# Optimization experiments

Measured on AMD Instinct MI355X. Metric: run time of the kernel, lower is better.

The kernel has to match this reference:

```python
import jax, jax.numpy as jnp
import numpy as np

SCALE_WEIGHT = 0.5 ** 0.5
B, C, T, S = 8, 512, 2048, 2048


def setup_inputs() -> dict:
    key = jax.random.key(0)
    ks = jax.random.split(key, 6)
    return {
        "base_target_emb": jax.random.normal(ks[0], (B, C, T, 1), dtype=jnp.float32),
        "input_from_dec": jax.random.normal(ks[1], (B, C, T, 1), dtype=jnp.float32),
        "encoder_out_top": jax.random.normal(ks[2], (B, C, S), dtype=jnp.float32),
        "encoder_out_combine": jax.random.normal(ks[3], (B, C, S), dtype=jnp.float32),
        "W": jax.random.normal(ks[4], (C, C), dtype=jnp.float32) * (1.0 / np.sqrt(C)),
        "b": jax.random.normal(ks[5], (C,), dtype=jnp.float32) * 0.01,
    }


def reference(base_target_emb, input_from_dec, encoder_out_top, encoder_out_combine, W, b):
    # seq_linear: per-token Linear over the channel dim. torch Linear: h = x @ W.T + b, W is [out,in]
    x = input_from_dec[..., 0]                                # [B,C,T]
    preatt = jnp.einsum('oc,bct->bot', W, x) + b[None, :, None]  # [B,C,T]
    target = (base_target_emb[..., 0] + preatt) * SCALE_WEIGHT   # [B,C,T]
    pre_attn = jnp.einsum('bct,bcs->bts', target, encoder_out_top)  # [B,T,S]
    attn = jax.nn.softmax(pre_attn, axis=2)                      # [B,T,S]
    ctx = jnp.einsum('bts,bcs->btc', attn, encoder_out_combine)  # [B,T,C]
    context_output = jnp.transpose(ctx, (0, 2, 1))[..., None]    # [B,C,T,1]
    return context_output, attn
```

## Files before the change

### kernel.cpp

```cpp
#include <hip/hip_runtime.h>
#include <cstddef>
#include <cstdint>

#define SCALE_WEIGHT 0.70710678118654752440f

static constexpr int B_ = 8, C_ = 512, T_ = 2048, S_ = 2048;
static constexpr size_t BCT_ = (size_t)B_ * C_ * T_;
static constexpr size_t BTS_ = (size_t)B_ * T_ * S_;

typedef _Float16 half_t;
typedef half_t half8  __attribute__((ext_vector_type(8)));
typedef half_t half4v __attribute__((ext_vector_type(4)));
typedef float  floatx4 __attribute__((ext_vector_type(4)));

__device__ __forceinline__ void gload_lds16(const void* g, void* l) {
    __builtin_amdgcn_global_load_lds(
        (const __attribute__((address_space(1))) void*)g,
        (__attribute__((address_space(3))) void*)l, 16, 0, 0);
}

__global__ __launch_bounds__(256) void transpose2_cvt_kernel(
    const float* __restrict__ x, const float* __restrict__ top,
    half_t* __restrict__ xT, half_t* __restrict__ topT)
{
    __shared__ float tile[64][65];
    const int z = blockIdx.z;
    const float* in = (z < 8) ? x : top;
    half_t* outp = (z < 8) ? xT : topT;
    const int b  = z & 7;
    const int r0 = blockIdx.y * 64, c0 = blockIdx.x * 64;
    const float* ib = in + (size_t)b * C_ * T_;
    half_t* ob = outp + (size_t)b * C_ * T_;
    const int t  = threadIdx.x;
    const int rr = t >> 4, cq = t & 15;
    #pragma unroll
    for (int i = 0; i < 4; ++i) {
        const int r = rr + i * 16;
        float4 v = *(const float4*)&ib[(size_t)(r0 + r) * T_ + c0 + cq * 4];
        tile[cq * 4 + 0][r] = v.x;
        tile[cq * 4 + 1][r] = v.y;
        tile[cq * 4 + 2][r] = v.z;
        tile[cq * 4 + 3][r] = v.w;
    }
    __syncthreads();
    const int cw = t >> 4, rq = (t & 15) * 4;
    #pragma unroll
    for (int i = 0; i < 4; ++i) {
        const int c = cw + i * 16;
        half4v h = {(half_t)tile[c][rq + 0], (half_t)tile[c][rq + 1],
                    (half_t)tile[c][rq + 2], (half_t)tile[c][rq + 3]};
        *(half4v*)&ob[(size_t)(c0 + c) * C_ + r0 + rq] = h;
    }
}

__global__ __launch_bounds__(256) void cvt2_f32_f16_kernel(
    const float* __restrict__ comb, half_t* __restrict__ combh,
    const float* __restrict__ W, half_t* __restrict__ Wh,
    int n4a, int n4tot)
{
    const int stride = gridDim.x * blockDim.x;
    for (int i = blockIdx.x * blockDim.x + threadIdx.x; i < n4tot; i += stride) {
        const float4* src; half4v* dst; int j;
        if (i < n4a) { src = (const float4*)comb; dst = (half4v*)combh; j = i; }
        else         { src = (const float4*)W;    dst = (half4v*)Wh;    j = i - n4a; }
        float4 v = src[j];
        dst[j] = (half4v){(half_t)v.x, (half_t)v.y, (half_t)v.z, (half_t)v.w};
    }
}

template<int MM, int NN, int KK, int EPI>
__global__ __launch_bounds__(256) void gemm32_kernel(
    const half_t* __restrict__ A, const half_t* __restrict__ Bm,
    size_t sA, size_t sB,
    float* __restrict__ outF, half_t* __restrict__ outH,
    const float* __restrict__ base, const float* __restrict__ bias,
    float* __restrict__ mArr, float* __restrict__ sArr,
    const float* __restrict__ fArr)
{
    constexpr int LDSSZ = (EPI == 1) ? 34816 : ((EPI == 2) ? 40960 : 32768);
    __shared__ __align__(128) char smem[LDSSZ];

    const int tid = threadIdx.x, lane = tid & 63, w = tid >> 6;
    const int wr = w >> 1, wc = w & 1;

    const int wgid = blockIdx.x;
    const int b = wgid & 7;
    const int tile = wgid >> 3;
    constexpr int NXT = NN / 128;
    constexpr int NMT = MM / 128;
    int m0, n0;
    if constexpr (EPI == 2) { n0 = (tile / NMT) * 128; m0 = (tile % NMT) * 128; }
    else                    { n0 = (tile % NXT) * 128; m0 = (tile / NXT) * 128; }

    const half_t* Ab = A  + (size_t)b * sA;
    const half_t* Bb = Bm + (size_t)b * sB;

    const int lr = lane >> 2, sl = lane & 3;
    const int ks = sl ^ (lr & 3);
    const half_t* aG0 = Ab + (size_t)(m0 + w * 32      + lr) * KK + ks * 8;
    const half_t* aG1 = Ab + (size_t)(m0 + w * 32 + 16 + lr) * KK + ks * 8;
    const half_t* bG0 = Bb + (size_t)(n0 + w * 32      + lr) * KK + ks * 8;
    const half_t* bG1 = Bb + (size_t)(n0 + w * 32 + 16 + lr) * KK + ks * 8;
    const int dOff0 = (w * 32) * 64, dOff1 = (w * 32 + 16) * 64;

    const int fr = lane & 15, kg = lane >> 4;
    const int q4 = kg * 4;
    int aoff[4], boff[4];
    #pragma unroll
    for (int mi = 0; mi < 4; ++mi) {
        const int m = wr * 64 + mi * 16 + fr;
        aoff[mi] = m * 64 + ((kg ^ (m & 3)) << 4);
    }
    #pragma unroll
    for (int nj = 0; nj < 4; ++nj) {
        const int n = wc * 64 + nj * 16 + fr;
        boff[nj] = n * 64 + ((kg ^ (n & 3)) << 4);
    }

    floatx4 acc[4][4];
    #pragma unroll
    for (int mi = 0; mi < 4; ++mi)
        #pragma unroll
        for (int nj = 0; nj < 4; ++nj)
            acc[mi][nj] = (floatx4){0.f, 0.f, 0.f, 0.f};

    auto STAGE = [&](int t, int pg) {
        const int k0 = t * 32;
        char* Ad = smem + pg * 8192;
        char* Bd = smem + 16384 + pg * 8192;
        gload_lds16(aG0 + k0, Ad + dOff0);
        gload_lds16(aG1 + k0, Ad + dOff1);
        gload_lds16(bG0 + k0, Bd + dOff0);
        gload_lds16(bG1 + k0, Bd + dOff1);
    };

    auto COMPUTE = [&](int pg, int t) {
        const char* Ar = smem + pg * 8192;
        const char* Br = smem + 16384 + pg * 8192;
        half8 af[4], bf[4];
        #pragma unroll
        for (int mi = 0; mi < 4; ++mi) af[mi] = *(const half8*)(Ar + aoff[mi]);
        #pragma unroll
        for (int nj = 0; nj < 4; ++nj) bf[nj] = *(const half8*)(Br + boff[nj]);
        if constexpr (EPI == 2) {
            const float* fls = (const float*)(smem + 32768);
            const int st = t >> 2;
            #pragma unroll
            for (int nj = 0; nj < 4; ++nj) {
                const half_t fh = (half_t)fls[st * 128 + wc * 64 + nj * 16 + fr];
                #pragma unroll
                for (int e = 0; e < 8; ++e) bf[nj][e] *= fh;
            }
        }
        #pragma unroll
        for (int mi = 0; mi < 4; ++mi)
            #pragma unroll
            for (int nj = 0; nj < 4; ++nj)
                acc[mi][nj] = __builtin_amdgcn_mfma_f32_16x16x32_f16(
                    af[mi], bf[nj], acc[mi][nj], 0, 0, 0);
    };

    if constexpr (EPI == 2) {
        const float* fB = fArr + (size_t)b * 16 * T_;
        #pragma unroll
        for (int c = 0; c < 8; ++c)
            gload_lds16(fB + (size_t)(2 * c + (lane >> 5)) * T_ + n0 + (lane & 31) * 4,
                        smem + 32768 + c * 1024);
    }
    constexpr int NT = KK / 32;
    STAGE(0, 0);
    int cur = 0;
    #pragma unroll 1
    for (int t = 0; t < NT - 1; ++t) {
        STAGE(t + 1, cur ^ 1);
        __builtin_amdgcn_sched_barrier(0);
        asm volatile("s_waitcnt vmcnt(4)" ::: "memory");
        __builtin_amdgcn_s_barrier();
        __builtin_amdgcn_sched_barrier(0);
        COMPUTE(cur, t);
        asm volatile("s_waitcnt lgkmcnt(0)" ::: "memory");
        __builtin_amdgcn_sched_barrier(0);
        __builtin_amdgcn_s_barrier();
        __builtin_amdgcn_sched_barrier(0);
        cur ^= 1;
    }
    asm volatile("s_waitcnt vmcnt(0)" ::: "memory");
    __builtin_amdgcn_s_barrier();
    __builtin_amdgcn_sched_barrier(0);
    COMPUTE(cur, NT - 1);

    if constexpr (EPI == 0) {
        half_t* Cb = outH + (size_t)b * ((size_t)MM * NN);
        #pragma unroll
        for (int nj = 0; nj < 4; ++nj) {
            const int col = n0 + wc * 64 + nj * 16 + fr;
            const float bn = bias[col];
            const float* bp = base + ((size_t)b * NN + col) * (size_t)MM;
            #pragma unroll
            for (int mi = 0; mi < 4; ++mi) {
                const int row = m0 + wr * 64 + mi * 16 + q4;
                #pragma unroll
                for (int r = 0; r < 4; ++r) {
                    float v = (acc[mi][nj][r] + bn + bp[row + r]) * SCALE_WEIGHT;
                    Cb[(size_t)(row + r) * NN + col] = (half_t)v;
                }
            }
        }
    } else if constexpr (EPI == 2) {
        float* Cb = outF + (size_t)b * ((size_t)MM * NN);
        #pragma unroll
        for (int mi = 0; mi < 4; ++mi) {
            const int row = m0 + wr * 64 + mi * 16 + q4;
            #pragma unroll
            for (int nj = 0; nj < 4; ++nj) {
                const int col = n0 + wc * 64 + nj * 16 + fr;
                #pragma unroll
                for (int r = 0; r < 4; ++r)
                    Cb[(size_t)(row + r) * NN + col] = acc[mi][nj][r];
            }
        }
    } else {
        __syncthreads();
        float* rmax = (float*)(smem + 32768);
        float* rsum = (float*)(smem + 32768 + 1024);

        #pragma unroll
        for (int mi = 0; mi < 4; ++mi)
            #pragma unroll
            for (int r = 0; r < 4; ++r) {
                float v = fmaxf(fmaxf(acc[mi][0][r], acc[mi][1][r]),
                                fmaxf(acc[mi][2][r], acc[mi][3][r]));
                v = fmaxf(v, __shfl_xor(v, 1));
                v = fmaxf(v, __shfl_xor(v, 2));
                v = fmaxf(v, __shfl_xor(v, 4));
                v = fmaxf(v, __shfl_xor(v, 8));
                if (fr == 0) rmax[wc * 128 + wr * 64 + mi * 16 + q4 + r] = v;
            }
        __syncthreads();

        #pragma unroll
        for (int mi = 0; mi < 4; ++mi)
            #pragma unroll
            for (int r = 0; r < 4; ++r) {
                const int row = wr * 64 + mi * 16 + q4 + r;
                const float mC = fmaxf(rmax[row], rmax[128 + row]);
                float s = 0.f;
                #pragma unroll
                for (int nj = 0; nj < 4; ++nj) {
                    const int col = wc * 64 + nj * 16 + fr;
                    float pv = __expf(acc[mi][nj][r] - mC);
                    s += pv;
                    *(half_t*)(smem + row * 256 + ((col * 2) ^ ((row & 7) << 4))) =
                        (half_t)pv;
                }
                s += __shfl_xor(s, 1);
                s += __shfl_xor(s, 2);
                s += __shfl_xor(s, 4);
                s += __shfl_xor(s, 8);
                if (fr == 0) rsum[wc * 128 + row] = s;
            }
        __syncthreads();

        if (tid < 128) {
            const float m = fmaxf(rmax[tid], rmax[128 + tid]);
            const float s = rsum[tid] + rsum[128 + tid];
            const size_t si = ((size_t)(b * 16 + (n0 >> 7))) * (size_t)MM + m0 + tid;
            mArr[si] = m;
            sArr[si] = s;
        }

        half_t* Pb = outH + ((size_t)b * MM + m0) * (size_t)NN + n0;
        const int rlo = tid >> 4, slot = tid & 15;
        #pragma unroll
        for (int pp = 0; pp < 8; ++pp) {
            const int row = pp * 16 + rlo;
            const int lb = row * 256 + ((slot * 16) ^ ((row & 7) << 4));
            half8 v = *(const half8*)(smem + lb);
            *(half8*)&Pb[(size_t)row * NN + slot * 8] = v;
        }
    }
}

__global__ __launch_bounds__(256) void kf_kernel(
    const float* __restrict__ mArr, const float* __restrict__ sArr,
    float* __restrict__ fArr)
{
    const int gid = blockIdx.x * 256 + threadIdx.x;
    const int b = gid >> 11, t = gid & 2047;
    float mv[16];
    float mfin = -3.0e38f;
    #pragma unroll
    for (int j = 0; j < 16; ++j) {
        mv[j] = mArr[((size_t)(b * 16 + j)) * T_ + t];
        mfin = fmaxf(mfin, mv[j]);
    }
    float sig = 0.f;
    #pragma unroll
    for (int j = 0; j < 16; ++j)
        sig += sArr[((size_t)(b * 16 + j)) * T_ + t] * __expf(mv[j] - mfin);
    const float inv = 1.f / sig;
    #pragma unroll
    for (int j = 0; j < 16; ++j)
        fArr[((size_t)(b * 16 + j)) * T_ + t] = __expf(mv[j] - mfin) * inv;
}

__global__ __launch_bounds__(256) void k3n_kernel(
    const half_t* __restrict__ P, const float* __restrict__ fArr,
    float* __restrict__ attnf)
{
    const int bid = blockIdx.x;
    const int b = bid >> 11, t = bid & 2047;
    const int tid = threadIdx.x;
    const float f = fArr[((size_t)(b * 16 + (tid >> 4))) * T_ + t];
    const size_t rb = (size_t)bid * S_ + tid * 8;
    half8 v = *(const half8*)&P[rb];
    float4 o0 = {(float)v[0] * f, (float)v[1] * f, (float)v[2] * f, (float)v[3] * f};
    float4 o1 = {(float)v[4] * f, (float)v[5] * f, (float)v[6] * f, (float)v[7] * f};
    *(float4*)&attnf[rb]     = o0;
    *(float4*)&attnf[rb + 4] = o1;
}

extern "C" void kernel_launch(void* const* d_in, const int* in_sizes, int n_in,
                              void* d_out, int out_size, void* d_ws, size_t ws_size,
                              hipStream_t stream) {
    const float* base = (const float*)d_in[0];
    const float* x    = (const float*)d_in[1];
    const float* top  = (const float*)d_in[2];
    const float* comb = (const float*)d_in[3];
    const float* W    = (const float*)d_in[4];
    const float* bias = (const float*)d_in[5];

    float* out   = (float*)d_out;
    float* ctx   = out;
    float* attnf = out + BCT_;

    half_t* xT   = (half_t*)d_out;
    half_t* topT = xT + BCT_;

    half_t* pws   = (half_t*)d_ws;
    half_t* combh = pws + BTS_;
    half_t* Wh    = combh + (size_t)B_ * C_ * S_;
    half_t* tgtT  = Wh + (size_t)C_ * C_;
    float*  mArr  = (float*)(tgtT + BCT_);
    float*  sArr  = mArr + (size_t)B_ * 16 * T_;
    float*  fArr  = sArr + (size_t)B_ * 16 * T_;

    transpose2_cvt_kernel<<<dim3(T_ / 64, C_ / 64, 16), 256, 0, stream>>>(x, top, xT, topT);
    {
        const int n4a = (int)((size_t)B_ * C_ * S_ / 4);
        const int n4tot = n4a + C_ * C_ / 4;
        cvt2_f32_f16_kernel<<<2048, 256, 0, stream>>>(comb, combh, W, Wh, n4a, n4tot);
    }

    gemm32_kernel<2048, 512, 512, 0><<<512, 256, 0, stream>>>(
        xT, Wh, (size_t)T_ * C_, 0,
        nullptr, tgtT, base, bias, nullptr, nullptr, nullptr);

    gemm32_kernel<2048, 2048, 512, 1><<<2048, 256, 0, stream>>>(
        tgtT, topT, (size_t)T_ * C_, (size_t)S_ * C_,
        nullptr, pws, nullptr, nullptr, mArr, sArr, nullptr);

    kf_kernel<<<64, 256, 0, stream>>>(mArr, sArr, fArr);

    k3n_kernel<<<B_ * T_, 256, 0, stream>>>(pws, fArr, attnf);

    gemm32_kernel<512, 2048, 2048, 2><<<512, 256, 0, stream>>>(
        combh, pws, (size_t)C_ * S_, (size_t)T_ * S_,
        ctx, nullptr, nullptr, nullptr, nullptr, nullptr, fArr);
}
```

Measured before the change: 235.2 us.

## Enlarge GEMM tiles to 512 threads with 4-stage LDS ring, merge prep kernels

The GEMM kernel now uses 512-thread workgroups with BN=256 and BM=128 or 256, which halves the softmax partial-statistics slices from 16 to 8 per row. The old double-buffered LDS loop is replaced by a 4-deep prefetch ring that needs only one barrier per K step, and MFMA sections are wrapped in s_setprio. The two conversion kernels are merged into one launch. Larger tiles raise data reuse, but they also raise LDS and register pressure and cut the number of workgroups, so occupancy may drop.

```diff
diff --git a/kernel.cpp b/kernel.cpp
--- a/kernel.cpp
+++ b/kernel.cpp
@@ -19,57 +19,58 @@
         (__attribute__((address_space(3))) void*)l, 16, 0, 0);
 }
 
-__global__ __launch_bounds__(256) void transpose2_cvt_kernel(
+__global__ __launch_bounds__(256) void pre_kernel(
     const float* __restrict__ x, const float* __restrict__ top,
-    half_t* __restrict__ xT, half_t* __restrict__ topT)
+    const float* __restrict__ comb, const float* __restrict__ W,
+    half_t* __restrict__ xT, half_t* __restrict__ topT,
+    half_t* __restrict__ combh, half_t* __restrict__ Wh)
 {
-    __shared__ float tile[64][65];
     const int z = blockIdx.z;
-    const float* in = (z < 8) ? x : top;
-    half_t* outp = (z < 8) ? xT : topT;
-    const int b  = z & 7;
-    const int r0 = blockIdx.y * 64, c0 = blockIdx.x * 64;
-    const float* ib = in + (size_t)b * C_ * T_;
-    half_t* ob = outp + (size_t)b * C_ * T_;
-    const int t  = threadIdx.x;
-    const int rr = t >> 4, cq = t & 15;
-    #pragma unroll
-    for (int i = 0; i < 4; ++i) {
-        const int r = rr + i * 16;
-        float4 v = *(const float4*)&ib[(size_t)(r0 + r) * T_ + c0 + cq * 4];
-        tile[cq * 4 + 0][r] = v.x;
-        tile[cq * 4 + 1][r] = v.y;
-        tile[cq * 4 + 2][r] = v.z;
-        tile[cq * 4 + 3][r] = v.w;
-    }
-    __syncthreads();
-    const int cw = t >> 4, rq = (t & 15) * 4;
-    #pragma unroll
-    for (int i = 0; i < 4; ++i) {
-        const int c = cw + i * 16;
-        half4v h = {(half_t)tile[c][rq + 0], (half_t)tile[c][rq + 1],
-                    (half_t)tile[c][rq + 2], (half_t)tile[c][rq + 3]};
-        *(half4v*)&ob[(size_t)(c0 + c) * C_ + r0 + rq] = h;
-    }
-}
-
-__global__ __launch_bounds__(256) void cvt2_f32_f16_kernel(
-    const float* __restrict__ comb, half_t* __restrict__ combh,
-    const float* __restrict__ W, half_t* __restrict__ Wh,
-    int n4a, int n4tot)
-{
-    const int stride = gridDim.x * blockDim.x;
-    for (int i = blockIdx.x * blockDim.x + threadIdx.x; i < n4tot; i += stride) {
-        const float4* src; half4v* dst; int j;
-        if (i < n4a) { src = (const float4*)comb; dst = (half4v*)combh; j = i; }
-        else         { src = (const float4*)W;    dst = (half4v*)Wh;    j = i - n4a; }
-        float4 v = src[j];
-        dst[j] = (half4v){(half_t)v.x, (half_t)v.y, (half_t)v.z, (half_t)v.w};
-    }
-}
-
-template<int MM, int NN, int KK, int EPI>
-__global__ __launch_bounds__(256) void gemm32_kernel(
+    if (z < 16) {
+        __shared__ float tile[64][65];
+        const float* in = (z < 8) ? x : top;
+        half_t* outp = (z < 8) ? xT : topT;
+        const int b  = z & 7;
+        const int r0 = blockIdx.y * 64, c0 = blockIdx.x * 64;
+        const float* ib = in + (size_t)b * C_ * T_;
+        half_t* ob = outp + (size_t)b * C_ * T_;
+        const int t  = threadIdx.x;
+        const int rr = t >> 4, cq = t & 15;
+        #pragma unroll
+        for (int i = 0; i < 4; ++i) {
+            const int r = rr + i * 16;
+            float4 v = *(const float4*)&ib[(size_t)(r0 + r) * T_ + c0 + cq * 4];
+            tile[cq * 4 + 0][r] = v.x;
+            tile[cq * 4 + 1][r] = v.y;
+            tile[cq * 4 + 2][r] = v.z;
+            tile[cq * 4 + 3][r] = v.w;
+        }
+        __syncthreads();
+        const int cw = t >> 4, rq = (t & 15) * 4;
+        #pragma unroll
+        for (int i = 0; i < 4; ++i) {
+            const int c = cw + i * 16;
+            half4v h = {(half_t)tile[c][rq + 0], (half_t)tile[c][rq + 1],
+                        (half_t)tile[c][rq + 2], (half_t)tile[c][rq + 3]};
+            *(half4v*)&ob[(size_t)(c0 + c) * C_ + r0 + rq] = h;
+        }
+    } else {
+        const int n4a = (int)((size_t)B_ * C_ * S_ / 4);
+        const int n4tot = n4a + C_ * C_ / 4;
+        const int planeT = 32 * 8 * 256;
+        for (int i = (blockIdx.y * 32 + blockIdx.x) * 256 + threadIdx.x;
+             i < n4tot; i += planeT) {
+            const float4* src; half4v* dst; int j;
+            if (i < n4a) { src = (const float4*)comb; dst = (half4v*)combh; j = i; }
+            else         { src = (const float4*)W;    dst = (half4v*)Wh;    j = i - n4a; }
+            float4 v = src[j];
+            dst[j] = (half4v){(half_t)v.x, (half_t)v.y, (half_t)v.z, (half_t)v.w};
+        }
+    }
+}
+
+template<int BM, int MM, int NN, int KK, int EPI>
+__global__ __launch_bounds__(512) void gemmv2_kernel(
     const half_t* __restrict__ A, const half_t* __restrict__ Bm,
     size_t sA, size_t sB,
     float* __restrict__ outF, half_t* __restrict__ outH,
@@ -77,117 +78,117 @@
     float* __restrict__ mArr, float* __restrict__ sArr,
     const float* __restrict__ fArr)
 {
-    constexpr int LDSSZ = (EPI == 1) ? 34816 : ((EPI == 2) ? 40960 : 32768);
+    constexpr int BN   = 256;
+    constexpr int AKT  = BM * 64;
+    constexpr int KTB  = (BM + BN) * 64;
+    constexpr int RING = 4 * KTB;
+    constexpr int MI   = BM / 32;
+    constexpr int NT   = KK / 32;
+    constexpr int POFF = 256 * 528;
+    constexpr int LDSSZ = (EPI == 1) ? (POFF + 8192)
+                        : (EPI == 2) ? (RING + 8192) : RING;
+    static_assert(LDSSZ >= RING || EPI == 1, "ring fit");
     __shared__ __align__(128) char smem[LDSSZ];
 
     const int tid = threadIdx.x, lane = tid & 63, w = tid >> 6;
-    const int wr = w >> 1, wc = w & 1;
+    const int wr = w >> 2, wc = w & 3;
+    const int fr = lane & 15, kg = lane >> 4, q4 = kg * 4;
 
     const int wgid = blockIdx.x;
     const int b = wgid & 7;
     const int tile = wgid >> 3;
-    constexpr int NXT = NN / 128;
-    constexpr int NMT = MM / 128;
     int m0, n0;
-    if constexpr (EPI == 2) { n0 = (tile / NMT) * 128; m0 = (tile % NMT) * 128; }
-    else                    { n0 = (tile % NXT) * 128; m0 = (tile / NXT) * 128; }
+    if constexpr (EPI == 2) {
+        m0 = (tile % (MM / BM)) * BM;
+        n0 = (tile / (MM / BM)) * BN;
+    } else {
+        n0 = (tile % (NN / BN)) * BN;
+        m0 = (tile / (NN / BN)) * BM;
+    }
 
     const half_t* Ab = A  + (size_t)b * sA;
     const half_t* Bb = Bm + (size_t)b * sB;
 
-    const int lr = lane >> 2, sl = lane & 3;
-    const int ks = sl ^ (lr & 3);
-    const half_t* aG0 = Ab + (size_t)(m0 + w * 32      + lr) * KK + ks * 8;
-    const half_t* aG1 = Ab + (size_t)(m0 + w * 32 + 16 + lr) * KK + ks * 8;
-    const half_t* bG0 = Bb + (size_t)(n0 + w * 32      + lr) * KK + ks * 8;
-    const half_t* bG1 = Bb + (size_t)(n0 + w * 32 + 16 + lr) * KK + ks * 8;
-    const int dOff0 = (w * 32) * 64, dOff1 = (w * 32 + 16) * 64;
-
-    const int fr = lane & 15, kg = lane >> 4;
-    const int q4 = kg * 4;
-    int aoff[4], boff[4];
-    #pragma unroll
-    for (int mi = 0; mi < 4; ++mi) {
-        const int m = wr * 64 + mi * 16 + fr;
+    const int rowr = w * 16 + (lane >> 2);
+    const int ks8  = (((lane & 3) ^ ((lane >> 2) & 3)) << 3);
+
+    auto STAGE = [&](int t) {
+        if (t >= NT) return;
+        char* bs = smem + (t & 3) * KTB;
+        const int k0 = t * 32;
+        #pragma unroll
+        for (int r = 0; r < BM / 128; ++r)
+            gload_lds16(Ab + (size_t)(m0 + r * 128 + rowr) * KK + k0 + ks8,
+                        bs + (r * 128 + w * 16) * 64);
+        #pragma unroll
+        for (int r = 0; r < BN / 128; ++r)
+            gload_lds16(Bb + (size_t)(n0 + r * 128 + rowr) * KK + k0 + ks8,
+                        bs + AKT + (r * 128 + w * 16) * 64);
+    };
+
+    int aoff[MI], boff[4];
+    #pragma unroll
+    for (int mi = 0; mi < MI; ++mi) {
+        const int m = wr * (BM / 2) + mi * 16 + fr;
         aoff[mi] = m * 64 + ((kg ^ (m & 3)) << 4);
     }
     #pragma unroll
     for (int nj = 0; nj < 4; ++nj) {
         const int n = wc * 64 + nj * 16 + fr;
-        boff[nj] = n * 64 + ((kg ^ (n & 3)) << 4);
-    }
-
-    floatx4 acc[4][4];
-    #pragma unroll
-    for (int mi = 0; mi < 4; ++mi)
+        boff[nj] = AKT + n * 64 + ((kg ^ (n & 3)) << 4);
+    }
+
+    floatx4 acc[MI][4];
+    #pragma unroll
+    for (int mi = 0; mi < MI; ++mi)
         #pragma unroll
         for (int nj = 0; nj < 4; ++nj)
             acc[mi][nj] = (floatx4){0.f, 0.f, 0.f, 0.f};
 
-    auto STAGE = [&](int t, int pg) {
-        const int k0 = t * 32;
-        char* Ad = smem + pg * 8192;
-        char* Bd = smem + 16384 + pg * 8192;
-        gload_lds16(aG0 + k0, Ad + dOff0);
-        gload_lds16(aG1 + k0, Ad + dOff1);
-        gload_lds16(bG0 + k0, Bd + dOff0);
-        gload_lds16(bG1 + k0, Bd + dOff1);
-    };
-
-    auto COMPUTE = [&](int pg, int t) {
-        const char* Ar = smem + pg * 8192;
-        const char* Br = smem + 16384 + pg * 8192;
-        half8 af[4], bf[4];
-        #pragma unroll
-        for (int mi = 0; mi < 4; ++mi) af[mi] = *(const half8*)(Ar + aoff[mi]);
-        #pragma unroll
-        for (int nj = 0; nj < 4; ++nj) bf[nj] = *(const half8*)(Br + boff[nj]);
+    if constexpr (EPI == 2) {
+        gload_lds16(fArr + ((size_t)b * 8 + w) * (size_t)NN + n0 + (lane << 2),
+                    smem + RING + w * 1024);
+    }
+    STAGE(0); STAGE(1); STAGE(2);
+
+    #pragma unroll 1
+    for (int t = 0; t < NT; ++t) {
+        if constexpr (EPI == 1) {
+            asm volatile("s_waitcnt vmcnt(8)" ::: "memory");
+        } else {
+            asm volatile("s_waitcnt vmcnt(6)" ::: "memory");
+        }
+        __builtin_amdgcn_s_barrier();
+        __builtin_amdgcn_sched_barrier(0);
+        STAGE(t + 3);
+        __builtin_amdgcn_sched_barrier(0);
+
+        const char* kb = smem + (t & 3) * KTB;
+        half8 bf[4];
+        #pragma unroll
+        for (int nj = 0; nj < 4; ++nj) bf[nj] = *(const half8*)(kb + boff[nj]);
         if constexpr (EPI == 2) {
-            const float* fls = (const float*)(smem + 32768);
-            const int st = t >> 2;
+            const float* fls = (const float*)(smem + RING);
+            const int st = t >> 3;
             #pragma unroll
             for (int nj = 0; nj < 4; ++nj) {
-                const half_t fh = (half_t)fls[st * 128 + wc * 64 + nj * 16 + fr];
+                const half_t fh = (half_t)fls[st * 256 + wc * 64 + nj * 16 + fr];
                 #pragma unroll
                 for (int e = 0; e < 8; ++e) bf[nj][e] *= fh;
             }
         }
-        #pragma unroll
-        for (int mi = 0; mi < 4; ++mi)
+        __builtin_amdgcn_s_setprio(1);
+        #pragma unroll
+        for (int mi = 0; mi < MI; ++mi) {
+            half8 af = *(const half8*)(kb + aoff[mi]);
             #pragma unroll
             for (int nj = 0; nj < 4; ++nj)
                 acc[mi][nj] = __builtin_amdgcn_mfma_f32_16x16x32_f16(
-                    af[mi], bf[nj], acc[mi][nj], 0, 0, 0);
-    };
-
-    if constexpr (EPI == 2) {
-        const float* fB = fArr + (size_t)b * 16 * T_;
-        #pragma unroll
-        for (int c = 0; c < 8; ++c)
-            gload_lds16(fB + (size_t)(2 * c + (lane >> 5)) * T_ + n0 + (lane & 31) * 4,
-                        smem + 32768 + c * 1024);
-    }
-    constexpr int NT = KK / 32;
-    STAGE(0, 0);
-    int cur = 0;
-    #pragma unroll 1
-    for (int t = 0; t < NT - 1; ++t) {
-        STAGE(t + 1, cur ^ 1);
+                    af, bf[nj], acc[mi][nj], 0, 0, 0);
+        }
+        __builtin_amdgcn_s_setprio(0);
         __builtin_amdgcn_sched_barrier(0);
-        asm volatile("s_waitcnt vmcnt(4)" ::: "memory");
-        __builtin_amdgcn_s_barrier();
-        __builtin_amdgcn_sched_barrier(0);
-        COMPUTE(cur, t);
-        asm volatile("s_waitcnt lgkmcnt(0)" ::: "memory");
-        __builtin_amdgcn_sched_barrier(0);
-        __builtin_amdgcn_s_barrier();
-        __builtin_amdgcn_sched_barrier(0);
-        cur ^= 1;
-    }
-    asm volatile("s_waitcnt vmcnt(0)" ::: "memory");
-    __builtin_amdgcn_s_barrier();
-    __builtin_amdgcn_sched_barrier(0);
-    COMPUTE(cur, NT - 1);
+    }
 
     if constexpr (EPI == 0) {
         half_t* Cb = outH + (size_t)b * ((size_t)MM * NN);
@@ -197,8 +198,8 @@
             const float bn = bias[col];
             const float* bp = base + ((size_t)b * NN + col) * (size_t)MM;
             #pragma unroll
-            for (int mi = 0; mi < 4; ++mi) {
-                const int row = m0 + wr * 64 + mi * 16 + q4;
+            for (int mi = 0; mi < MI; ++mi) {
+                const int row = m0 + wr * (BM / 2) + mi * 16 + q4;
                 #pragma unroll
                 for (int r = 0; r < 4; ++r) {
                     float v = (acc[mi][nj][r] + bn + bp[row + r]) * SCALE_WEIGHT;
@@ -209,8 +210,8 @@
     } else if constexpr (EPI == 2) {
         float* Cb = outF + (size_t)b * ((size_t)MM * NN);
         #pragma unroll
-        for (int mi = 0; mi < 4; ++mi) {
-            const int row = m0 + wr * 64 + mi * 16 + q4;
+        for (int mi = 0; mi < MI; ++mi) {
+            const int row = m0 + wr * (BM / 2) + mi * 16 + q4;
             #pragma unroll
             for (int nj = 0; nj < 4; ++nj) {
                 const int col = n0 + wc * 64 + nj * 16 + fr;
@@ -220,12 +221,13 @@
             }
         }
     } else {
+        asm volatile("s_waitcnt vmcnt(0)" ::: "memory");
         __syncthreads();
-        float* rmax = (float*)(smem + 32768);
-        float* rsum = (float*)(smem + 32768 + 1024);
-
-        #pragma unroll
-        for (int mi = 0; mi < 4; ++mi)
+        float* rmax = (float*)(smem + POFF);
+        float* rsum = rmax + 1024;
+
+        #pragma unroll
+        for (int mi = 0; mi < MI; ++mi)
             #pragma unroll
             for (int r = 0; r < 4; ++r) {
                 float v = fmaxf(fmaxf(acc[mi][0][r], acc[mi][1][r]),
@@ -234,49 +236,50 @@
                 v = fmaxf(v, __shfl_xor(v, 2));
                 v = fmaxf(v, __shfl_xor(v, 4));
                 v = fmaxf(v, __shfl_xor(v, 8));
-                if (fr == 0) rmax[wc * 128 + wr * 64 + mi * 16 + q4 + r] = v;
+                if (fr == 0)
+                    rmax[wc * 256 + wr * 128 + mi * 16 + q4 + r] = v;
             }
         __syncthreads();
 
         #pragma unroll
-        for (int mi = 0; mi < 4; ++mi)
+        for (int mi = 0; mi < MI; ++mi)
             #pragma unroll
             for (int r = 0; r < 4; ++r) {
-                const int row = wr * 64 + mi * 16 + q4 + r;
-                const float mC = fmaxf(rmax[row], rmax[128 + row]);
+                const int row = wr * 128 + mi * 16 + q4 + r;
+                const float mC = fmaxf(fmaxf(rmax[row], rmax[256 + row]),
+                                       fmaxf(rmax[512 + row], rmax[768 + row]));
                 float s = 0.f;
                 #pragma unroll
                 for (int nj = 0; nj < 4; ++nj) {
                     const int col = wc * 64 + nj * 16 + fr;
                     float pv = __expf(acc[mi][nj][r] - mC);
                     s += pv;
-                    *(half_t*)(smem + row * 256 + ((col * 2) ^ ((row & 7) << 4))) =
-                        (half_t)pv;
+                    *(half_t*)(smem + row * 528 + col * 2) = (half_t)pv;
                 }
                 s += __shfl_xor(s, 1);
                 s += __shfl_xor(s, 2);
                 s += __shfl_xor(s, 4);
                 s += __shfl_xor(s, 8);
-                if (fr == 0) rsum[wc * 128 + row] = s;
+                if (fr == 0) rsum[wc * 256 + row] = s;
             }
         __syncthreads();
 
-        if (tid < 128) {
-            const float m = fmaxf(rmax[tid], rmax[128 + tid]);
-            const float s = rsum[tid] + rsum[128 + tid];
-            const size_t si = ((size_t)(b * 16 + (n0 >> 7))) * (size_t)MM + m0 + tid;
+        if (tid < 256) {
+            const float m = fmaxf(fmaxf(rmax[tid], rmax[256 + tid]),
+                                  fmaxf(rmax[512 + tid], rmax[768 + tid]));
+            const float s = rsum[tid] + rsum[256 + tid] +
+                            rsum[512 + tid] + rsum[768 + tid];
+            const size_t si = ((size_t)(b * 8 + (n0 >> 8))) * (size_t)MM + m0 + tid;
             mArr[si] = m;
             sArr[si] = s;
         }
 
-        half_t* Pb = outH + ((size_t)b * MM + m0) * (size_t)NN + n0;
-        const int rlo = tid >> 4, slot = tid & 15;
-        #pragma unroll
-        for (int pp = 0; pp < 8; ++pp) {
-            const int row = pp * 16 + rlo;
-            const int lb = row * 256 + ((slot * 16) ^ ((row & 7) << 4));
-            half8 v = *(const half8*)(smem + lb);
-            *(half8*)&Pb[(size_t)row * NN + slot * 8] = v;
+        const int prow = tid >> 1, ph = tid & 1;
+        const size_t gb = ((size_t)b * MM + m0 + prow) * (size_t)NN + n0 + ph * 128;
+        #pragma unroll
+        for (int j = 0; j < 16; ++j) {
+            half8 v = *(const half8*)(smem + prow * 528 + ph * 256 + j * 16);
+            *(half8*)&outH[gb + j * 8] = v;
         }
     }
 }
@@ -287,21 +290,21 @@
 {
     const int gid = blockIdx.x * 256 + threadIdx.x;
     const int b = gid >> 11, t = gid & 2047;
-    float mv[16];
+    float mv[8];
     float mfin = -3.0e38f;
     #pragma unroll
-    for (int j = 0; j < 16; ++j) {
-        mv[j] = mArr[((size_t)(b * 16 + j)) * T_ + t];
+    for (int j = 0; j < 8; ++j) {
+        mv[j] = mArr[((size_t)(b * 8 + j)) * T_ + t];
         mfin = fmaxf(mfin, mv[j]);
     }
     float sig = 0.f;
     #pragma unroll
-    for (int j = 0; j < 16; ++j)
-        sig += sArr[((size_t)(b * 16 + j)) * T_ + t] * __expf(mv[j] - mfin);
+    for (int j = 0; j < 8; ++j)
+        sig += sArr[((size_t)(b * 8 + j)) * T_ + t] * __expf(mv[j] - mfin);
     const float inv = 1.f / sig;
     #pragma unroll
-    for (int j = 0; j < 16; ++j)
-        fArr[((size_t)(b * 16 + j)) * T_ + t] = __expf(mv[j] - mfin) * inv;
+    for (int j = 0; j < 8; ++j)
+        fArr[((size_t)(b * 8 + j)) * T_ + t] = __expf(mv[j] - mfin) * inv;
 }
 
 __global__ __launch_bounds__(256) void k3n_kernel(
@@ -311,7 +314,7 @@
     const int bid = blockIdx.x;
     const int b = bid >> 11, t = bid & 2047;
     const int tid = threadIdx.x;
-    const float f = fArr[((size_t)(b * 16 + (tid >> 4))) * T_ + t];
+    const float f = fArr[((size_t)(b * 8 + (tid >> 5))) * T_ + t];
     const size_t rb = (size_t)bid * S_ + tid * 8;
     half8 v = *(const half8*)&P[rb];
     float4 o0 = {(float)v[0] * f, (float)v[1] * f, (float)v[2] * f, (float)v[3] * f};
@@ -342,21 +345,17 @@
     half_t* Wh    = combh + (size_t)B_ * C_ * S_;
     half_t* tgtT  = Wh + (size_t)C_ * C_;
     float*  mArr  = (float*)(tgtT + BCT_);
-    float*  sArr  = mArr + (size_t)B_ * 16 * T_;
-    float*  fArr  = sArr + (size_t)B_ * 16 * T_;
-
-    transpose2_cvt_kernel<<<dim3(T_ / 64, C_ / 64, 16), 256, 0, stream>>>(x, top, xT, topT);
-    {
-        const int n4a = (int)((size_t)B_ * C_ * S_ / 4);
-        const int n4tot = n4a + C_ * C_ / 4;
-        cvt2_f32_f16_kernel<<<2048, 256, 0, stream>>>(comb, combh, W, Wh, n4a, n4tot);
-    }
-
-    gemm32_kernel<2048, 512, 512, 0><<<512, 256, 0, stream>>>(
+    float*  sArr  = mArr + (size_t)B_ * 8 * T_;
+    float*  fArr  = sArr + (size_t)B_ * 8 * T_;
+
+    pre_kernel<<<dim3(32, 8, 17), 256, 0, stream>>>(
+        x, top, comb, W, xT, topT, combh, Wh);
+
+    gemmv2_kernel<128, 2048, 512, 512, 0><<<256, 512, 0, stream>>>(
         xT, Wh, (size_t)T_ * C_, 0,
         nullptr, tgtT, base, bias, nullptr, nullptr, nullptr);
 
-    gemm32_kernel<2048, 2048, 512, 1><<<2048, 256, 0, stream>>>(
+    gemmv2_kernel<256, 2048, 2048, 512, 1><<<512, 512, 0, stream>>>(
         tgtT, topT, (size_t)T_ * C_, (size_t)S_ * C_,
         nullptr, pws, nullptr, nullptr, mArr, sArr, nullptr);
 
@@ -364,7 +363,7 @@
 
     k3n_kernel<<<B_ * T_, 256, 0, stream>>>(pws, fArr, attnf);
 
-    gemm32_kernel<512, 2048, 2048, 2><<<512, 256, 0, stream>>>(
+    gemmv2_kernel<128, 512, 2048, 2048, 2><<<256, 512, 0, stream>>>(
         combh, pws, (size_t)C_ * S_, (size_t)T_ * S_,
         ctx, nullptr, nullptr, nullptr, nullptr, nullptr, fArr);
 }
```

New measurement: 241.4 us. 1.03x slower.

## Deepen GEMM K-tile to 64 and merge preprocessing kernels into one launch

Applied to the files above, without the earlier changes.

The GEMM template now stages 64-wide K slices instead of 32, using 16KB LDS buffers per operand with an 8-way XOR swizzle. This halves the number of barrier and wait iterations per tile and lets each stage issue more loads in flight. The transpose/convert and elementwise convert kernels are merged into one launch, and the softmax P-tile write-back is remapped so each thread writes 64 contiguous halves. LDS use roughly doubles (up to about 72KB), which may reduce occupancy.

```diff
diff --git a/kernel.cpp b/kernel.cpp
--- a/kernel.cpp
+++ b/kernel.cpp
@@ -19,57 +19,58 @@
         (__attribute__((address_space(3))) void*)l, 16, 0, 0);
 }
 
-__global__ __launch_bounds__(256) void transpose2_cvt_kernel(
+__global__ __launch_bounds__(256) void pre_kernel(
     const float* __restrict__ x, const float* __restrict__ top,
-    half_t* __restrict__ xT, half_t* __restrict__ topT)
+    const float* __restrict__ comb, const float* __restrict__ W,
+    half_t* __restrict__ xT, half_t* __restrict__ topT,
+    half_t* __restrict__ combh, half_t* __restrict__ Wh)
 {
-    __shared__ float tile[64][65];
     const int z = blockIdx.z;
-    const float* in = (z < 8) ? x : top;
-    half_t* outp = (z < 8) ? xT : topT;
-    const int b  = z & 7;
-    const int r0 = blockIdx.y * 64, c0 = blockIdx.x * 64;
-    const float* ib = in + (size_t)b * C_ * T_;
-    half_t* ob = outp + (size_t)b * C_ * T_;
-    const int t  = threadIdx.x;
-    const int rr = t >> 4, cq = t & 15;
-    #pragma unroll
-    for (int i = 0; i < 4; ++i) {
-        const int r = rr + i * 16;
-        float4 v = *(const float4*)&ib[(size_t)(r0 + r) * T_ + c0 + cq * 4];
-        tile[cq * 4 + 0][r] = v.x;
-        tile[cq * 4 + 1][r] = v.y;
-        tile[cq * 4 + 2][r] = v.z;
-        tile[cq * 4 + 3][r] = v.w;
-    }
-    __syncthreads();
-    const int cw = t >> 4, rq = (t & 15) * 4;
-    #pragma unroll
-    for (int i = 0; i < 4; ++i) {
-        const int c = cw + i * 16;
-        half4v h = {(half_t)tile[c][rq + 0], (half_t)tile[c][rq + 1],
-                    (half_t)tile[c][rq + 2], (half_t)tile[c][rq + 3]};
-        *(half4v*)&ob[(size_t)(c0 + c) * C_ + r0 + rq] = h;
-    }
-}
-
-__global__ __launch_bounds__(256) void cvt2_f32_f16_kernel(
-    const float* __restrict__ comb, half_t* __restrict__ combh,
-    const float* __restrict__ W, half_t* __restrict__ Wh,
-    int n4a, int n4tot)
-{
-    const int stride = gridDim.x * blockDim.x;
-    for (int i = blockIdx.x * blockDim.x + threadIdx.x; i < n4tot; i += stride) {
-        const float4* src; half4v* dst; int j;
-        if (i < n4a) { src = (const float4*)comb; dst = (half4v*)combh; j = i; }
-        else         { src = (const float4*)W;    dst = (half4v*)Wh;    j = i - n4a; }
-        float4 v = src[j];
-        dst[j] = (half4v){(half_t)v.x, (half_t)v.y, (half_t)v.z, (half_t)v.w};
+    if (z < 16) {
+        __shared__ float tile[64][65];
+        const float* in = (z < 8) ? x : top;
+        half_t* outp = (z < 8) ? xT : topT;
+        const int b  = z & 7;
+        const int r0 = blockIdx.y * 64, c0 = blockIdx.x * 64;
+        const float* ib = in + (size_t)b * C_ * T_;
+        half_t* ob = outp + (size_t)b * C_ * T_;
+        const int t  = threadIdx.x;
+        const int rr = t >> 4, cq = t & 15;
+        #pragma unroll
+        for (int i = 0; i < 4; ++i) {
+            const int r = rr + i * 16;
+            float4 v = *(const float4*)&ib[(size_t)(r0 + r) * T_ + c0 + cq * 4];
+            tile[cq * 4 + 0][r] = v.x;
+            tile[cq * 4 + 1][r] = v.y;
+            tile[cq * 4 + 2][r] = v.z;
+            tile[cq * 4 + 3][r] = v.w;
+        }
+        __syncthreads();
+        const int cw = t >> 4, rq = (t & 15) * 4;
+        #pragma unroll
+        for (int i = 0; i < 4; ++i) {
+            const int c = cw + i * 16;
+            half4v h = {(half_t)tile[c][rq + 0], (half_t)tile[c][rq + 1],
+                        (half_t)tile[c][rq + 2], (half_t)tile[c][rq + 3]};
+            *(half4v*)&ob[(size_t)(c0 + c) * C_ + r0 + rq] = h;
+        }
+    } else {
+        const int n4a = (int)((size_t)B_ * C_ * S_ / 4);
+        const int n4tot = n4a + C_ * C_ / 4;
+        const int planeT = 32 * 8 * 256;
+        for (int i = (blockIdx.y * 32 + blockIdx.x) * 256 + threadIdx.x;
+             i < n4tot; i += planeT) {
+            const float4* src; half4v* dst; int j;
+            if (i < n4a) { src = (const float4*)comb; dst = (half4v*)combh; j = i; }
+            else         { src = (const float4*)W;    dst = (half4v*)Wh;    j = i - n4a; }
+            float4 v = src[j];
+            dst[j] = (half4v){(half_t)v.x, (half_t)v.y, (half_t)v.z, (half_t)v.w};
+        }
     }
 }
 
 template<int MM, int NN, int KK, int EPI>
-__global__ __launch_bounds__(256) void gemm32_kernel(
+__global__ __launch_bounds__(256) void gemm64_kernel(
     const half_t* __restrict__ A, const half_t* __restrict__ Bm,
     size_t sA, size_t sB,
     float* __restrict__ outF, half_t* __restrict__ outH,
@@ -77,44 +78,52 @@
     float* __restrict__ mArr, float* __restrict__ sArr,
     const float* __restrict__ fArr)
 {
-    constexpr int LDSSZ = (EPI == 1) ? 34816 : ((EPI == 2) ? 40960 : 32768);
+    constexpr int NT = KK >> 6;
+    constexpr int LDSSZ = (EPI == 1) ? 67584 : ((EPI == 2) ? 73728 : 65536);
     __shared__ __align__(128) char smem[LDSSZ];
 
-    const int tid = threadIdx.x, lane = tid & 63, w = tid >> 6;
+    const int tid  = threadIdx.x;
+    const int lane = tid & 63, w = tid >> 6;
     const int wr = w >> 1, wc = w & 1;
 
     const int wgid = blockIdx.x;
     const int b = wgid & 7;
     const int tile = wgid >> 3;
-    constexpr int NXT = NN / 128;
-    constexpr int NMT = MM / 128;
     int m0, n0;
-    if constexpr (EPI == 2) { n0 = (tile / NMT) * 128; m0 = (tile % NMT) * 128; }
-    else                    { n0 = (tile % NXT) * 128; m0 = (tile / NXT) * 128; }
+    if constexpr (EPI == 2) {
+        m0 = (tile % (MM / 128)) * 128;
+        n0 = (tile / (MM / 128)) * 128;
+    } else {
+        n0 = (tile % (NN / 128)) * 128;
+        m0 = (tile / (NN / 128)) * 128;
+    }
 
     const half_t* Ab = A  + (size_t)b * sA;
     const half_t* Bb = Bm + (size_t)b * sB;
 
-    const int lr = lane >> 2, sl = lane & 3;
-    const int ks = sl ^ (lr & 3);
-    const half_t* aG0 = Ab + (size_t)(m0 + w * 32      + lr) * KK + ks * 8;
-    const half_t* aG1 = Ab + (size_t)(m0 + w * 32 + 16 + lr) * KK + ks * 8;
-    const half_t* bG0 = Bb + (size_t)(n0 + w * 32      + lr) * KK + ks * 8;
-    const half_t* bG1 = Bb + (size_t)(n0 + w * 32 + 16 + lr) * KK + ks * 8;
-    const int dOff0 = (w * 32) * 64, dOff1 = (w * 32 + 16) * 64;
-
-    const int fr = lane & 15, kg = lane >> 4;
-    const int q4 = kg * 4;
+    const int lr = lane >> 3;
+    const int sw = (lane & 7) ^ lr;
+    const half_t* aG[4]; const half_t* bG[4];
+    int dOff[4];
+    #pragma unroll
+    for (int i = 0; i < 4; ++i) {
+        const int r = w * 32 + i * 8 + lr;
+        aG[i] = Ab + (size_t)(m0 + r) * KK + sw * 8;
+        bG[i] = Bb + (size_t)(n0 + r) * KK + sw * 8;
+        dOff[i] = (w * 32 + i * 8) * 128;
+    }
+
+    const int fr = lane & 15, kg = lane >> 4, q4 = kg * 4;
     int aoff[4], boff[4];
     #pragma unroll
     for (int mi = 0; mi < 4; ++mi) {
         const int m = wr * 64 + mi * 16 + fr;
-        aoff[mi] = m * 64 + ((kg ^ (m & 3)) << 4);
+        aoff[mi] = m * 128 + ((kg ^ (m & 7)) << 4);
     }
     #pragma unroll
     for (int nj = 0; nj < 4; ++nj) {
         const int n = wc * 64 + nj * 16 + fr;
-        boff[nj] = n * 64 + ((kg ^ (n & 3)) << 4);
+        boff[nj] = n * 128 + ((kg ^ (n & 7)) << 4);
     }
 
     floatx4 acc[4][4];
@@ -125,56 +134,60 @@
             acc[mi][nj] = (floatx4){0.f, 0.f, 0.f, 0.f};
 
     auto STAGE = [&](int t, int pg) {
-        const int k0 = t * 32;
-        char* Ad = smem + pg * 8192;
-        char* Bd = smem + 16384 + pg * 8192;
-        gload_lds16(aG0 + k0, Ad + dOff0);
-        gload_lds16(aG1 + k0, Ad + dOff1);
-        gload_lds16(bG0 + k0, Bd + dOff0);
-        gload_lds16(bG1 + k0, Bd + dOff1);
+        const int k0 = t * 64;
+        char* Ad = smem + pg * 16384;
+        char* Bd = smem + 32768 + pg * 16384;
+        #pragma unroll
+        for (int i = 0; i < 4; ++i) {
+            gload_lds16(aG[i] + k0, Ad + dOff[i]);
+            gload_lds16(bG[i] + k0, Bd + dOff[i]);
+        }
     };
 
     auto COMPUTE = [&](int pg, int t) {
-        const char* Ar = smem + pg * 8192;
-        const char* Br = smem + 16384 + pg * 8192;
-        half8 af[4], bf[4];
-        #pragma unroll
-        for (int mi = 0; mi < 4; ++mi) af[mi] = *(const half8*)(Ar + aoff[mi]);
-        #pragma unroll
-        for (int nj = 0; nj < 4; ++nj) bf[nj] = *(const half8*)(Br + boff[nj]);
-        if constexpr (EPI == 2) {
-            const float* fls = (const float*)(smem + 32768);
-            const int st = t >> 2;
-            #pragma unroll
-            for (int nj = 0; nj < 4; ++nj) {
-                const half_t fh = (half_t)fls[st * 128 + wc * 64 + nj * 16 + fr];
-                #pragma unroll
-                for (int e = 0; e < 8; ++e) bf[nj][e] *= fh;
-            }
-        }
-        #pragma unroll
-        for (int mi = 0; mi < 4; ++mi)
+        const char* Ar = smem + pg * 16384;
+        const char* Br = smem + 32768 + pg * 16384;
+        #pragma unroll
+        for (int kk = 0; kk < 2; ++kk) {
+            half8 af[4], bf[4];
+            #pragma unroll
+            for (int mi = 0; mi < 4; ++mi)
+                af[mi] = *(const half8*)(Ar + (aoff[mi] ^ (kk << 6)));
             #pragma unroll
             for (int nj = 0; nj < 4; ++nj)
-                acc[mi][nj] = __builtin_amdgcn_mfma_f32_16x16x32_f16(
-                    af[mi], bf[nj], acc[mi][nj], 0, 0, 0);
+                bf[nj] = *(const half8*)(Br + (boff[nj] ^ (kk << 6)));
+            if constexpr (EPI == 2) {
+                const float* fls = (const float*)(smem + 65536);
+                const int st = t >> 1;
+                #pragma unroll
+                for (int nj = 0; nj < 4; ++nj) {
+                    const half_t fh = (half_t)fls[st * 128 + wc * 64 + nj * 16 + fr];
+                    #pragma unroll
+                    for (int e = 0; e < 8; ++e) bf[nj][e] *= fh;
+                }
+            }
+            #pragma unroll
+            for (int mi = 0; mi < 4; ++mi)
+                #pragma unroll
+                for (int nj = 0; nj < 4; ++nj)
+                    acc[mi][nj] = __builtin_amdgcn_mfma_f32_16x16x32_f16(
+                        af[mi], bf[nj], acc[mi][nj], 0, 0, 0);
+        }
     };
 
     if constexpr (EPI == 2) {
-        const float* fB = fArr + (size_t)b * 16 * T_;
+        const float* fB = fArr + (size_t)b * 16 * NN;
         #pragma unroll
         for (int c = 0; c < 8; ++c)
-            gload_lds16(fB + (size_t)(2 * c + (lane >> 5)) * T_ + n0 + (lane & 31) * 4,
-                        smem + 32768 + c * 1024);
-    }
-    constexpr int NT = KK / 32;
+            gload_lds16(fB + (size_t)(2 * c + (lane >> 5)) * NN + n0 + (lane & 31) * 4,
+                        smem + 65536 + c * 1024);
+    }
     STAGE(0, 0);
     int cur = 0;
     #pragma unroll 1
     for (int t = 0; t < NT - 1; ++t) {
         STAGE(t + 1, cur ^ 1);
-        __builtin_amdgcn_sched_barrier(0);
-        asm volatile("s_waitcnt vmcnt(4)" ::: "memory");
+        asm volatile("s_waitcnt vmcnt(8)" ::: "memory");
         __builtin_amdgcn_s_barrier();
         __builtin_amdgcn_sched_barrier(0);
         COMPUTE(cur, t);
@@ -221,8 +234,8 @@
         }
     } else {
         __syncthreads();
-        float* rmax = (float*)(smem + 32768);
-        float* rsum = (float*)(smem + 32768 + 1024);
+        float* rmax = (float*)(smem + 65536);
+        float* rsum = (float*)(smem + 66560);
 
         #pragma unroll
         for (int mi = 0; mi < 4; ++mi)
@@ -269,14 +282,13 @@
             sArr[si] = s;
         }
 
-        half_t* Pb = outH + ((size_t)b * MM + m0) * (size_t)NN + n0;
-        const int rlo = tid >> 4, slot = tid & 15;
-        #pragma unroll
-        for (int pp = 0; pp < 8; ++pp) {
-            const int row = pp * 16 + rlo;
-            const int lb = row * 256 + ((slot * 16) ^ ((row & 7) << 4));
-            half8 v = *(const half8*)(smem + lb);
-            *(half8*)&Pb[(size_t)row * NN + slot * 8] = v;
+        const int prow = tid >> 1, ph = tid & 1;
+        half_t* Pb = outH + ((size_t)b * MM + m0 + prow) * (size_t)NN + n0 + ph * 64;
+        #pragma unroll
+        for (int j = 0; j < 8; ++j) {
+            half8 v = *(const half8*)(smem + prow * 256 +
+                                      ((ph * 128 + j * 16) ^ ((prow & 7) << 4)));
+            *(half8*)&Pb[j * 8] = v;
         }
     }
 }
@@ -345,18 +357,14 @@
     float*  sArr  = mArr + (size_t)B_ * 16 * T_;
     float*  fArr  = sArr + (size_t)B_ * 16 * T_;
 
-    transpose2_cvt_kernel<<<dim3(T_ / 64, C_ / 64, 16), 256, 0, stream>>>(x, top, xT, topT);
-    {
-        const int n4a = (int)((size_t)B_ * C_ * S_ / 4);
-        const int n4tot = n4a + C_ * C_ / 4;
-        cvt2_f32_f16_kernel<<<2048, 256, 0, stream>>>(comb, combh, W, Wh, n4a, n4tot);
-    }
-
-    gemm32_kernel<2048, 512, 512, 0><<<512, 256, 0, stream>>>(
+    pre_kernel<<<dim3(32, 8, 17), 256, 0, stream>>>(
+        x, top, comb, W, xT, topT, combh, Wh);
+
+    gemm64_kernel<2048, 512, 512, 0><<<512, 256, 0, stream>>>(
         xT, Wh, (size_t)T_ * C_, 0,
         nullptr, tgtT, base, bias, nullptr, nullptr, nullptr);
 
-    gemm32_kernel<2048, 2048, 512, 1><<<2048, 256, 0, stream>>>(
+    gemm64_kernel<2048, 2048, 512, 1><<<2048, 256, 0, stream>>>(
         tgtT, topT, (size_t)T_ * C_, (size_t)S_ * C_,
         nullptr, pws, nullptr, nullptr, mArr, sArr, nullptr);
 
@@ -364,7 +372,7 @@
 
     k3n_kernel<<<B_ * T_, 256, 0, stream>>>(pws, fArr, attnf);
 
-    gemm32_kernel<512, 2048, 2048, 2><<<512, 256, 0, stream>>>(
+    gemm64_kernel<512, 2048, 2048, 2><<<512, 256, 0, stream>>>(
         combh, pws, (size_t)C_ * S_, (size_t)T_ * S_,
         ctx, nullptr, nullptr, nullptr, nullptr, nullptr, fArr);
 }
```

After: 248.5 us. 1.06x slower.
